# Optimization experiments

Measured on AMD Instinct MI355X. Metric: run time of the kernel, lower is better.

The kernel has to match this reference:

```python
import jax, jax.numpy as jnp
import numpy as np

D = 768

def setup_inputs() -> dict:
    key = jax.random.key(0)
    ks = jax.random.split(key, 12)
    inp = {
        "text_embeddings": jax.random.normal(ks[0], (8, 512, D), dtype=jnp.float32),
        "kb_emb": jax.random.normal(ks[1], (200000, D), dtype=jnp.float32),
        "W_ret": jax.random.normal(ks[2], (D, D), dtype=jnp.float32) * 0.02,
        "b_ret": jax.random.normal(ks[3], (D,), dtype=jnp.float32) * 0.02,
        "Ws1": jax.random.normal(ks[4], (2 * D, D), dtype=jnp.float32) * 0.02,
        "bs1": jax.random.normal(ks[5], (D,), dtype=jnp.float32) * 0.02,
        "Ws2": jax.random.normal(ks[6], (D, 1), dtype=jnp.float32) * 0.02,
        "bs2": jax.random.normal(ks[7], (1,), dtype=jnp.float32) * 0.02,
        "mention_sent": jax.random.randint(ks[8], (256,), 0, 8, dtype=jnp.int32),
        "mention_start": jax.random.randint(ks[9], (256,), 0, 480, dtype=jnp.int32),
        "mention_len": jax.random.randint(ks[10], (256,), 0, 31, dtype=jnp.int32),
        "top_k": 100,
    }
    return inp


def reference(text_embeddings, kb_emb, W_ret, b_ret, Ws1, bs1, Ws2, bs2,
              mention_sent, mention_start, mention_len, top_k):
    S = text_embeddings.shape[1]
    pos = jnp.arange(S, dtype=jnp.int32)
    # inclusive span [start, start+len] -> mask [M, S]
    mask = (pos[None, :] >= mention_start[:, None]) & (pos[None, :] <= (mention_start + mention_len)[:, None])
    maskf = mask.astype(text_embeddings.dtype)
    sent = text_embeddings[mention_sent]                       # [M, S, D]
    mention_emb = jnp.einsum('msd,ms->md', sent, maskf) / maskf.sum(1, keepdims=True)

    # entity_retriever linear, then KB dot-product retrieval of top 2k candidates
    query = mention_emb @ W_ret.T + b_ret                      # [M, D]
    sims = query @ kb_emb.T                                    # [M, N]
    _, cand_idx = jax.lax.top_k(sims, 2 * top_k)               # [M, 2k]
    cand_embs = kb_emb[cand_idx]                               # [M, 2k, D]

    # candidate_scorer: Linear(2D->D) on concat(mention, cand) + ReLU + Linear(D->1) + Sigmoid
    m_part = mention_emb @ Ws1[:D]                             # [M, D]
    c_part = jnp.einsum('mkd,de->mke', cand_embs, Ws1[D:])     # [M, 2k, D]
    h = jax.nn.relu(m_part[:, None, :] + c_part + bs1)
    scores = jax.nn.sigmoid(jnp.einsum('mke,eo->mko', h, Ws2)[..., 0] + bs2[0])  # [M, 2k]

    top_scores, ti = jax.lax.top_k(scores, top_k)              # [M, k]
    top_kb_idx = jnp.take_along_axis(cand_idx, ti, axis=1)
    return top_scores, top_kb_idx
```

## Files before the change

kernel.cpp:

```cpp
#include <hip/hip_runtime.h>
#include <cfloat>
#include <cmath>
#include <cstdint>

#define DD 768
#define MM 256
#define NKB 200000
#define SLEN 512
#define KK 200
#define TOPK 100
#define SURV_CAP 1024
#define RESC 232
#define THRC 2.70f
#define MAXMARK 32768
#define DELTA 4e-5
#define NET 12

typedef __attribute__((ext_vector_type(8))) short bf16x8;
typedef __attribute__((ext_vector_type(4))) float f32x4;

__device__ __forceinline__ unsigned short f2bf_rne(float x) {
  unsigned u = __float_as_uint(x);
  unsigned r = (u + 0x7FFFu + ((u >> 16) & 1u)) >> 16;
  return (unsigned short)r;
}
__device__ __forceinline__ float bf2f(unsigned short us) {
  return __uint_as_float(((unsigned)us) << 16);
}
__device__ __forceinline__ void splitbf(float x, unsigned short& hi, unsigned short& lo) {
  hi = f2bf_rne(x);
  lo = f2bf_rne(x - bf2f(hi));
}

__global__ __launch_bounds__(256) void k_prepT(
    const float* __restrict__ Wret, float* __restrict__ WretT) {
  __shared__ float tile[64][65];
  int e0 = blockIdx.x * 64, d0 = blockIdx.y * 64;
  int tid = threadIdx.x;
  int r = tid >> 6, cc = tid & 63;
  for (int i = 0; i < 64; i += 4)
    tile[r + i][cc] = Wret[(size_t)(e0 + r + i) * DD + d0 + cc];
  __syncthreads();
  for (int i = 0; i < 64; i += 4)
    WretT[(size_t)(d0 + r + i) * DD + e0 + cc] = tile[cc][r + i];
}

__global__ __launch_bounds__(256) void k_front(
    const float* __restrict__ text, const int* __restrict__ msent,
    const int* __restrict__ mstart, const int* __restrict__ mlen,
    const float* __restrict__ WretT, const float* __restrict__ bret,
    const float* __restrict__ Ws1,
    double* __restrict__ q64, unsigned short* __restrict__ qb16,
    float* __restrict__ tthr, double* __restrict__ mp64,
    float* __restrict__ mp32) {
  int m = blockIdx.x;
  __shared__ double sme[DD];
  __shared__ float snorm[256];
  int tid = threadIdx.x;
  {
    int sent = msent[m], st = mstart[m], ln = mlen[m];
    const float* base = text + (size_t)sent * SLEN * DD;
    for (int d = tid; d < DD; d += 256) {
      double acc = 0.0;
      for (int s = st; s <= st + ln; ++s) acc += (double)base[(size_t)s * DD + d];
      sme[d] = acc / (double)(ln + 1);
    }
  }
  __syncthreads();
  float nloc = 0.f;
  for (int e = tid; e < DD; e += 256) {
    double aq = (double)bret[e];
    double amp = 0.0;
    for (int d = 0; d < DD; ++d) {
      double md = sme[d];
      aq  += md * (double)WretT[(size_t)d * DD + e];
      amp += md * (double)Ws1[(size_t)d * DD + e];
    }
    q64[(size_t)m * DD + e] = aq;
    qb16[(size_t)m * DD + e] = f2bf_rne((float)aq);
    mp64[(size_t)m * DD + e] = amp;
    mp32[(size_t)m * DD + e] = (float)amp;
    nloc += (float)(aq * aq);
  }
  snorm[tid] = nloc; __syncthreads();
  for (int s = 128; s > 0; s >>= 1) {
    if (tid < s) snorm[tid] += snorm[tid + s];
    __syncthreads();
  }
  if (tid == 0) tthr[m] = THRC * sqrtf(snorm[0]);
}

__global__ __launch_bounds__(256) void k_prep(
    const float* __restrict__ Ws1, unsigned short* __restrict__ Bth,
    unsigned short* __restrict__ Btl) {
  int e = blockIdx.x;
  for (int k = threadIdx.x; k < DD; k += 256) {
    float x = Ws1[(size_t)(DD + k) * DD + e];
    unsigned short hi, lo;
    splitbf(x, hi, lo);
    Bth[(size_t)e * DD + k] = hi;
    Btl[(size_t)e * DD + k] = lo;
  }
}

__global__ __launch_bounds__(512) void k_sims_mfma(
    const unsigned short* __restrict__ qb, const float* __restrict__ kb,
    const float* __restrict__ tthr, int* __restrict__ gcnt,
    uint2* __restrict__ gcand) {
  __shared__ unsigned short Bs[2][64 * 64];
  __shared__ float sthr[256];
  int n0 = blockIdx.x * 64;
  int tid = threadIdx.x;
  int lane = tid & 63, w = tid >> 6;
  int h = lane >> 4, c = lane & 15;
  if (tid < 256) sthr[tid] = tthr[tid];
  f32x4 acc[2][4] = {};
  const int brow = n0 + (tid >> 3);
  const int bg   = tid & 7;
  const int bwoff = ((tid >> 3) * 128 + bg * 16) ^ (((tid >> 3) & 7) << 4);
  auto ldB = [&](int k0, float4 &d0, float4 &d1) {
    const float* s = kb + (size_t)brow * DD + k0 + bg * 8;
    d0 = *(const float4*)(s);
    d1 = *(const float4*)(s + 4);
  };
  auto stB = [&](int buf, const float4 &v0, const float4 &v1) {
    uint4 p;
    p.x = (unsigned)f2bf_rne(v0.x) | ((unsigned)f2bf_rne(v0.y) << 16);
    p.y = (unsigned)f2bf_rne(v0.z) | ((unsigned)f2bf_rne(v0.w) << 16);
    p.z = (unsigned)f2bf_rne(v1.x) | ((unsigned)f2bf_rne(v1.y) << 16);
    p.w = (unsigned)f2bf_rne(v1.z) | ((unsigned)f2bf_rne(v1.w) << 16);
    *(uint4*)((char*)Bs + buf * 8192 + bwoff) = p;
  };
  const unsigned short* qa0 = qb + (size_t)(w * 32 + c) * DD;
  const unsigned short* qa1 = qb + (size_t)(w * 32 + 16 + c) * DD;
  float4 c0, c1, p1a, p1b, p2a, p2b;
  ldB(0, c0, c1);
  stB(0, c0, c1);
  ldB(64, p1a, p1b);
  ldB(128, p2a, p2b);
  __syncthreads();
#pragma unroll
  for (int s = 0; s < 12; ++s) {
    int cur = s & 1;
    int k0 = s * 64;
    if (s + 1 < 12) stB(cur ^ 1, p1a, p1b);
    p1a = p2a; p1b = p2b;
    if (s + 3 < 12) ldB((s + 3) * 64, p2a, p2b);
    bf16x8 a00 = *(const bf16x8*)(qa0 + k0 + h * 8);
    bf16x8 a10 = *(const bf16x8*)(qa1 + k0 + h * 8);
    bf16x8 a01 = *(const bf16x8*)(qa0 + k0 + 32 + h * 8);
    bf16x8 a11 = *(const bf16x8*)(qa1 + k0 + 32 + h * 8);
#pragma unroll
    for (int nf = 0; nf < 4; ++nf) {
      int n = nf * 16 + c;
      int off = (n * 128 + h * 16) ^ ((n & 7) << 4);
      bf16x8 b = *(bf16x8*)((char*)Bs + cur * 8192 + off);
      acc[0][nf] = __builtin_amdgcn_mfma_f32_16x16x32_bf16(a00, b, acc[0][nf], 0, 0, 0);
      acc[1][nf] = __builtin_amdgcn_mfma_f32_16x16x32_bf16(a10, b, acc[1][nf], 0, 0, 0);
    }
#pragma unroll
    for (int nf = 0; nf < 4; ++nf) {
      int n = nf * 16 + c;
      int off = (n * 128 + 64 + h * 16) ^ ((n & 7) << 4);
      bf16x8 b = *(bf16x8*)((char*)Bs + cur * 8192 + off);
      acc[0][nf] = __builtin_amdgcn_mfma_f32_16x16x32_bf16(a01, b, acc[0][nf], 0, 0, 0);
      acc[1][nf] = __builtin_amdgcn_mfma_f32_16x16x32_bf16(a11, b, acc[1][nf], 0, 0, 0);
    }
    __syncthreads();
  }
#pragma unroll
  for (int mf = 0; mf < 2; ++mf)
#pragma unroll
    for (int nf = 0; nf < 4; ++nf)
#pragma unroll
      for (int r = 0; r < 4; ++r) {
        int row = w * 32 + mf * 16 + h * 4 + r;
        int col = n0 + nf * 16 + c;
        float v = acc[mf][nf][r];
        if (v > sthr[row]) {
          int p = atomicAdd(&gcnt[row], 1);
          if (p < SURV_CAP) gcand[(size_t)row * SURV_CAP + p] = make_uint2(__float_as_uint(v), (unsigned)col);
        }
      }
}

__global__ __launch_bounds__(256) void k_select(
    const uint2* __restrict__ gcand, const int* __restrict__ gcnt,
    const float* __restrict__ kb, const double* __restrict__ q64,
    int* __restrict__ cidx) {
  int m = blockIdx.x;
  __shared__ float skf[SURV_CAP];
  __shared__ int   sidx[SURV_CAP];
  __shared__ double sq[DD];
  __shared__ double skey[256];
  __shared__ int    skidx[256];
  int tid = threadIdx.x;
  int cnt = gcnt[m]; if (cnt > SURV_CAP) cnt = SURV_CAP;
  for (int d = tid; d < DD; d += 256) sq[d] = q64[(size_t)m * DD + d];
  for (int i = tid; i < SURV_CAP; i += 256) {
    if (i < cnt) {
      uint2 v = gcand[(size_t)m * SURV_CAP + i];
      skf[i] = __uint_as_float(v.x);
      sidx[i] = (int)v.y;
    } else { skf[i] = -FLT_MAX; sidx[i] = 0x7fffffff; }
  }
  __syncthreads();
  for (int k = 2; k <= SURV_CAP; k <<= 1) {
    for (int j = k >> 1; j > 0; j >>= 1) {
      for (int i = tid; i < SURV_CAP; i += 256) {
        int l = i ^ j;
        if (l > i) {
          float ka = skf[i], kb2 = skf[l];
          int ia = sidx[i], ib = sidx[l];
          bool lBefore = (kb2 > ka) || (kb2 == ka && ib < ia);
          bool iBefore = (ka > kb2) || (ka == kb2 && ia < ib);
          bool dir = ((i & k) == 0);
          bool sw = dir ? lBefore : iBefore;
          if (sw) { skf[i] = kb2; skf[l] = ka; sidx[i] = ib; sidx[l] = ia; }
        }
      }
      __syncthreads();
    }
  }
  int lane = tid & 63, wv = tid >> 6;
  for (int cpos = wv; cpos < RESC; cpos += 4) {
    int ci = sidx[cpos];
    double s;
    if (ci < NKB) {
      const float* krow = kb + (size_t)ci * DD;
      double acc = 0.0;
      for (int d = lane; d < DD; d += 64) acc += sq[d] * (double)krow[d];
      for (int off2 = 32; off2 > 0; off2 >>= 1) acc += __shfl_down(acc, off2, 64);
      s = acc;
    } else s = -INFINITY;
    if (lane == 0) { skey[cpos] = s; skidx[cpos] = ci; }
  }
  if (tid >= RESC && tid < 256) { skey[tid] = -INFINITY; skidx[tid] = 0x7fffffff; }
  __syncthreads();
  for (int k = 2; k <= 256; k <<= 1) {
    for (int j = k >> 1; j > 0; j >>= 1) {
      int i = tid, l = i ^ j;
      if (l > i) {
        double ka = skey[i], kb2 = skey[l];
        int ia = skidx[i], ib = skidx[l];
        bool lBefore = (kb2 > ka) || (kb2 == ka && ib < ia);
        bool iBefore = (ka > kb2) || (ka == kb2 && ia < ib);
        bool dir = ((i & k) == 0);
        bool sw = dir ? lBefore : iBefore;
        if (sw) { skey[i] = kb2; skey[l] = ka; skidx[i] = ib; skidx[l] = ia; }
      }
      __syncthreads();
    }
  }
  for (int cc = tid; cc < KK; cc += 256) {
    int v = skidx[cc];
    cidx[(size_t)m * KK + cc] = (v < NKB) ? v : 0;
  }
}

__global__ __launch_bounds__(256) void k_score2(
    const float* __restrict__ kb, const int* __restrict__ cidx,
    const float* __restrict__ mp32, const unsigned short* __restrict__ Bth,
    const unsigned short* __restrict__ Btl, const float* __restrict__ bs1,
    const float* __restrict__ Ws2, float* __restrict__ gpart) {
  __shared__ unsigned short Ah[256 * 32], Al[256 * 32];
  __shared__ unsigned short Bh[64 * 32], Bl[64 * 32];
  __shared__ float smp[3][64], sb1v[64], sw2v[64];
  __shared__ int srow[256];
  int p = blockIdx.x;
  int x = p & 7, j = p >> 3;
  int ct = x + 8 * (j / NET), et = j % NET;
  int r0 = ct * 256, e0 = et * 64;
  int tid = threadIdx.x, lane = tid & 63, w = tid >> 6;
  int h = lane >> 4, c = lane & 15;
  srow[tid] = cidx[r0 + tid];
  int m0 = r0 / KK;
  int mm1 = (m0 + 1 < MM) ? m0 + 1 : MM - 1;
  int mm2 = (m0 + 2 < MM) ? m0 + 2 : MM - 1;
  if (tid < 64) {
    smp[0][tid] = mp32[(size_t)m0 * DD + e0 + tid];
    smp[1][tid] = mp32[(size_t)mm1 * DD + e0 + tid];
    smp[2][tid] = mp32[(size_t)mm2 * DD + e0 + tid];
    sb1v[tid] = bs1[e0 + tid];
    sw2v[tid] = Ws2[e0 + tid];
  }
  __syncthreads();
  const float* aaddr[8];
#pragma unroll
  for (int it = 0; it < 8; ++it) {
    int idx = tid + it * 256;
    int rr = idx >> 3, f4 = idx & 7;
    aaddr[it] = kb + (size_t)srow[rr] * DD + f4 * 4;
  }
  const int be = tid >> 2, bk8 = tid & 3;
  const unsigned short* bhaddr = Bth + (size_t)(e0 + be) * DD + bk8 * 8;
  const unsigned short* bladdr = Btl + (size_t)(e0 + be) * DD + bk8 * 8;
  float4 pa[8];
  uint4 pbh, pbl;
#pragma unroll
  for (int it = 0; it < 8; ++it) pa[it] = *(const float4*)(aaddr[it]);
  pbh = *(const uint4*)(bhaddr);
  pbl = *(const uint4*)(bladdr);
  f32x4 acc[4][4] = {};
  for (int k0 = 0; k0 < DD; k0 += 32) {
    __syncthreads();
#pragma unroll
    for (int it = 0; it < 8; ++it) {
      int idx = tid + it * 256;
      int rr = idx >> 3, f4 = idx & 7;
      float4 v = pa[it];
      unsigned short h0, h1, h2, h3, l0, l1, l2, l3;
      splitbf(v.x, h0, l0); splitbf(v.y, h1, l1);
      splitbf(v.z, h2, l2); splitbf(v.w, h3, l3);
      uint2 ph, pl;
      ph.x = (unsigned)h0 | ((unsigned)h1 << 16); ph.y = (unsigned)h2 | ((unsigned)h3 << 16);
      pl.x = (unsigned)l0 | ((unsigned)l1 << 16); pl.y = (unsigned)l2 | ((unsigned)l3 << 16);
      int off = (rr * 64 + f4 * 8) ^ ((rr & 7) << 4);
      *(uint2*)((char*)Ah + off) = ph;
      *(uint2*)((char*)Al + off) = pl;
    }
    {
      int off = (be * 64 + bk8 * 16) ^ ((be & 7) << 4);
      *(uint4*)((char*)Bh + off) = pbh;
      *(uint4*)((char*)Bl + off) = pbl;
    }
    if (k0 + 32 < DD) {
#pragma unroll
      for (int it = 0; it < 8; ++it) pa[it] = *(const float4*)(aaddr[it] + k0 + 32);
      pbh = *(const uint4*)(bhaddr + k0 + 32);
      pbl = *(const uint4*)(bladdr + k0 + 32);
    }
    __syncthreads();
    bf16x8 ah[4], al[4];
#pragma unroll
    for (int mf = 0; mf < 4; ++mf) {
      int rr = w * 64 + mf * 16 + c;
      int off = (rr * 64 + h * 16) ^ ((rr & 7) << 4);
      ah[mf] = *(bf16x8*)((char*)Ah + off);
      al[mf] = *(bf16x8*)((char*)Al + off);
    }
#pragma unroll
    for (int nf = 0; nf < 4; ++nf) {
      int e = nf * 16 + c;
      int off = (e * 64 + h * 16) ^ ((e & 7) << 4);
      bf16x8 bh = *(bf16x8*)((char*)Bh + off);
      bf16x8 bl = *(bf16x8*)((char*)Bl + off);
#pragma unroll
      for (int mf = 0; mf < 4; ++mf) {
        acc[mf][nf] = __builtin_amdgcn_mfma_f32_16x16x32_bf16(ah[mf], bh, acc[mf][nf], 0, 0, 0);
        acc[mf][nf] = __builtin_amdgcn_mfma_f32_16x16x32_bf16(ah[mf], bl, acc[mf][nf], 0, 0, 0);
        acc[mf][nf] = __builtin_amdgcn_mfma_f32_16x16x32_bf16(al[mf], bh, acc[mf][nf], 0, 0, 0);
      }
    }
  }
  int bnd1 = (m0 + 1) * KK, bnd2 = (m0 + 2) * KK;
#pragma unroll
  for (int mf = 0; mf < 4; ++mf) {
    float zp[4] = {0.f, 0.f, 0.f, 0.f};
#pragma unroll
    for (int nf = 0; nf < 4; ++nf) {
      int el = nf * 16 + c;
      float b1v = sb1v[el], w2v = sw2v[el];
#pragma unroll
      for (int r = 0; r < 4; ++r) {
        int rowg = r0 + w * 64 + mf * 16 + h * 4 + r;
        int sel = (rowg >= bnd1) + (rowg >= bnd2);
        float hh = acc[mf][nf][r] + smp[sel][el] + b1v;
        if (hh > 0.f) zp[r] += hh * w2v;
      }
    }
#pragma unroll
    for (int r = 0; r < 4; ++r) {
      float v = zp[r];
      v += __shfl_xor(v, 1, 64);
      v += __shfl_xor(v, 2, 64);
      v += __shfl_xor(v, 4, 64);
      v += __shfl_xor(v, 8, 64);
      if (c == 0)
        gpart[(size_t)(r0 + w * 64 + mf * 16 + h * 4 + r) * NET + et] = v;
    }
  }
}

__global__ __launch_bounds__(256) void k_mark(
    const float* __restrict__ gpart, const float* __restrict__ bs2,
    double* __restrict__ z64, int* __restrict__ marks, int* __restrict__ mcnt) {
  int m = blockIdx.x;
  __shared__ double sk[256];
  __shared__ int sp[256];
  __shared__ int flag[256];
  int tid = threadIdx.x;
  flag[tid] = 0;
  if (tid < KK) {
    double s = 0.0;
#pragma unroll
    for (int i = 0; i < NET; ++i) s += (double)gpart[(size_t)(m * KK + tid) * NET + i];
    s += (double)bs2[0];
    z64[(size_t)m * KK + tid] = s;
    sk[tid] = s; sp[tid] = tid;
  } else { sk[tid] = -INFINITY; sp[tid] = 0x7fffffff; }
  __syncthreads();
  for (int k = 2; k <= 256; k <<= 1) {
    for (int j = k >> 1; j > 0; j >>= 1) {
      int i = tid, l = i ^ j;
      if (l > i) {
        double ka = sk[i], kb2 = sk[l];
        int ia = sp[i], ib = sp[l];
        bool lBefore = (kb2 > ka) || (kb2 == ka && ib < ia);
        bool iBefore = (ka > kb2) || (ka == kb2 && ia < ib);
        bool dir = ((i & k) == 0);
        bool sw = dir ? lBefore : iBefore;
        if (sw) { sk[i] = kb2; sk[l] = ka; sp[i] = ib; sp[l] = ia; }
      }
      __syncthreads();
    }
  }
  if (tid <= 120) {
    if (sk[tid] - sk[tid + 1] < DELTA) {
      flag[tid] = 1;
      atomicExch(&flag[tid + 1], 1);
    }
  }
  __syncthreads();
  if (tid <= 121 && flag[tid]) {
    int p = atomicAdd(mcnt, 1);
    if (p < MAXMARK) marks[p] = m * KK + sp[tid];
  }
}

__global__ __launch_bounds__(256) void k_rescore(
    const float* __restrict__ kb, const int* __restrict__ cidx,
    const double* __restrict__ mp64, const float* __restrict__ Ws1,
    const float* __restrict__ bs1, const float* __restrict__ Ws2,
    const float* __restrict__ bs2, const int* __restrict__ marks,
    const int* __restrict__ mcnt, double* __restrict__ z64) {
  int cnt = *mcnt; if (cnt > MAXMARK) cnt = MAXMARK;
  __shared__ float sc[DD];
  __shared__ double sred[256];
  int tid = threadIdx.x;
  for (int it = blockIdx.x; it < cnt; it += gridDim.x) {
    int r = marks[it];
    int m = r / KK;
    int row = cidx[r];
    for (int d = tid; d < DD; d += 256) sc[d] = kb[(size_t)row * DD + d];
    __syncthreads();
    double pz = 0.0;
    for (int e = tid; e < DD; e += 256) {
      double a = 0.0;
      for (int d = 0; d < DD; ++d) a += (double)sc[d] * (double)Ws1[(size_t)(DD + d) * DD + e];
      double hv = mp64[(size_t)m * DD + e] + a + (double)bs1[e];
      if (hv > 0) pz += hv * (double)Ws2[e];
    }
    sred[tid] = pz; __syncthreads();
    for (int s = 128; s > 0; s >>= 1) { if (tid < s) sred[tid] += sred[tid + s]; __syncthreads(); }
    if (tid == 0) z64[r] = sred[0] + (double)bs2[0];
    __syncthreads();
  }
}

__global__ __launch_bounds__(256) void k_final(
    const double* __restrict__ z64, const int* __restrict__ cidx, float* __restrict__ out) {
  int m = blockIdx.x;
  __shared__ double sk[256];
  __shared__ int sp[256];
  int tid = threadIdx.x;
  if (tid < KK) { sk[tid] = z64[(size_t)m * KK + tid]; sp[tid] = tid; }
  else { sk[tid] = -INFINITY; sp[tid] = 0x7fffffff; }
  __syncthreads();
  for (int k = 2; k <= 256; k <<= 1) {
    for (int j = k >> 1; j > 0; j >>= 1) {
      int i = tid, l = i ^ j;
      if (l > i) {
        double ka = sk[i], kb2 = sk[l];
        int ia = sp[i], ib = sp[l];
        bool lBefore = (kb2 > ka) || (kb2 == ka && ib < ia);
        bool iBefore = (ka > kb2) || (ka == kb2 && ia < ib);
        bool dir = ((i & k) == 0);
        bool sw = dir ? lBefore : iBefore;
        if (sw) { sk[i] = kb2; sk[l] = ka; sp[i] = ib; sp[l] = ia; }
      }
      __syncthreads();
    }
  }
  if (tid < TOPK) {
    double z = sk[tid];
    out[(size_t)m * TOPK + tid] = (float)(1.0 / (1.0 + exp(-z)));
    out[(size_t)MM * TOPK + (size_t)m * TOPK + tid] = (float)cidx[(size_t)m * KK + sp[tid]];
  }
}

extern "C" void kernel_launch(void* const* d_in, const int* in_sizes, int n_in,
                              void* d_out, int out_size, void* d_ws, size_t ws_size,
                              hipStream_t stream) {
  const float* text  = (const float*)d_in[0];
  const float* kb    = (const float*)d_in[1];
  const float* Wret  = (const float*)d_in[2];
  const float* bret  = (const float*)d_in[3];
  const float* Ws1   = (const float*)d_in[4];
  const float* bs1   = (const float*)d_in[5];
  const float* Ws2   = (const float*)d_in[6];
  const float* bs2   = (const float*)d_in[7];
  const int* msent   = (const int*)d_in[8];
  const int* mstart  = (const int*)d_in[9];
  const int* mlen    = (const int*)d_in[10];
  float* out = (float*)d_out;

  char* ws = (char*)d_ws;
  size_t off = 0;
  auto alloc = [&](size_t bytes) -> void* {
    void* p = ws + off;
    off = (off + bytes + 255) & ~(size_t)255;
    return p;
  };
  double* q64  = (double*)alloc((size_t)MM * DD * 8);
  unsigned short* qb16 = (unsigned short*)alloc((size_t)MM * DD * 2);
  float*  tthr = (float*) alloc((size_t)MM * 4);
  double* mp64 = (double*)alloc((size_t)MM * DD * 8);
  float*  mp32 = (float*) alloc((size_t)MM * DD * 4);
  int*    cidx = (int*)   alloc((size_t)MM * KK * 4);
  double* z64  = (double*)alloc((size_t)MM * KK * 8);
  float*  gpart = (float*)alloc((size_t)MM * KK * NET * 4);
  int*    marks = (int*)  alloc((size_t)MAXMARK * 4);
  int*    mcnt  = (int*)  alloc(256);
  int*    gcnt  = (int*)  alloc((size_t)MM * 4);
  uint2*  gcand = (uint2*)alloc((size_t)MM * SURV_CAP * 8);
  unsigned short* Bth = (unsigned short*)alloc((size_t)DD * DD * 2);
  unsigned short* Btl = (unsigned short*)alloc((size_t)DD * DD * 2);
  float*  WretT = (float*)alloc((size_t)DD * DD * 4);
  (void)ws_size;

  dim3 gt(DD / 64, DD / 64);
  k_prepT<<<gt, 256, 0, stream>>>(Wret, WretT);
  k_prep<<<DD, 256, 0, stream>>>(Ws1, Bth, Btl);
  k_front<<<MM, 256, 0, stream>>>(text, msent, mstart, mlen, WretT, bret, Ws1,
                                  q64, qb16, tthr, mp64, mp32);

  hipMemsetAsync(gcnt, 0, (size_t)MM * 4, stream);
  k_sims_mfma<<<NKB / 64, 512, 0, stream>>>(qb16, kb, tthr, gcnt, gcand);
  k_select<<<MM, 256, 0, stream>>>(gcand, gcnt, kb, q64, cidx);

  k_score2<<<(MM * KK / 256) * NET, 256, 0, stream>>>(kb, cidx, mp32, Bth, Btl, bs1, Ws2, gpart);
  hipMemsetAsync(mcnt, 0, 4, stream);
  k_mark<<<MM, 256, 0, stream>>>(gpart, bs2, z64, marks, mcnt);
  k_rescore<<<2048, 256, 0, stream>>>(kb, cidx, mp64, Ws1, bs1, Ws2, bs2, marks, mcnt, z64);
  k_final<<<MM, 256, 0, stream>>>(z64, cidx, out);
}
```

Before: 1.287 ms.

## Halve sims block to 4 waves, each covering 64 query rows with 32-wide K steps

The KB similarity GEMM block shrinks from 8 waves to 4, and each wave now covers 64 mention rows (4 M-fragments) instead of 32. The K loop steps by 32 instead of 64, halving the shared-memory B tile. Each B fragment read from LDS now feeds four MFMAs instead of two, which raises register reuse and cuts LDS traffic per FLOP. The cost is more accumulator registers per thread, and twice as many barrier-separated iterations.

```diff
diff --git a/kernel.cpp b/kernel.cpp
--- a/kernel.cpp
+++ b/kernel.cpp
@@ -103,23 +103,23 @@
   }
 }
 
-__global__ __launch_bounds__(512) void k_sims_mfma(
+__global__ __launch_bounds__(256) void k_sims_mfma(
     const unsigned short* __restrict__ qb, const float* __restrict__ kb,
     const float* __restrict__ tthr, int* __restrict__ gcnt,
     uint2* __restrict__ gcand) {
-  __shared__ unsigned short Bs[2][64 * 64];
+  __shared__ unsigned short Bs[2][64 * 32];
   __shared__ float sthr[256];
   int n0 = blockIdx.x * 64;
   int tid = threadIdx.x;
   int lane = tid & 63, w = tid >> 6;
   int h = lane >> 4, c = lane & 15;
-  if (tid < 256) sthr[tid] = tthr[tid];
-  f32x4 acc[2][4] = {};
-  const int brow = n0 + (tid >> 3);
-  const int bg   = tid & 7;
-  const int bwoff = ((tid >> 3) * 128 + bg * 16) ^ (((tid >> 3) & 7) << 4);
+  sthr[tid] = tthr[tid];
+  f32x4 acc[4][4] = {};
+  const int brow = n0 + (tid >> 2);
+  const int bkg  = (tid & 3) * 8;
+  const int bwoff = ((tid >> 2) * 64 + bkg * 2) ^ (((tid >> 2) & 7) << 4);
   auto ldB = [&](int k0, float4 &d0, float4 &d1) {
-    const float* s = kb + (size_t)brow * DD + k0 + bg * 8;
+    const float* s = kb + (size_t)brow * DD + k0 + bkg;
     d0 = *(const float4*)(s);
     d1 = *(const float4*)(s + 4);
   };
@@ -129,52 +129,47 @@
     p.y = (unsigned)f2bf_rne(v0.z) | ((unsigned)f2bf_rne(v0.w) << 16);
     p.z = (unsigned)f2bf_rne(v1.x) | ((unsigned)f2bf_rne(v1.y) << 16);
     p.w = (unsigned)f2bf_rne(v1.z) | ((unsigned)f2bf_rne(v1.w) << 16);
-    *(uint4*)((char*)Bs + buf * 8192 + bwoff) = p;
+    *(uint4*)((char*)Bs + buf * 4096 + bwoff) = p;
   };
-  const unsigned short* qa0 = qb + (size_t)(w * 32 + c) * DD;
-  const unsigned short* qa1 = qb + (size_t)(w * 32 + 16 + c) * DD;
+  const unsigned short* qa[4];
+#pragma unroll
+  for (int mf = 0; mf < 4; ++mf)
+    qa[mf] = qb + (size_t)(w * 64 + mf * 16 + c) * DD;
   float4 c0, c1, p1a, p1b, p2a, p2b;
   ldB(0, c0, c1);
   stB(0, c0, c1);
-  ldB(64, p1a, p1b);
-  ldB(128, p2a, p2b);
-  __syncthreads();
-#pragma unroll
-  for (int s = 0; s < 12; ++s) {
+  ldB(32, p1a, p1b);
+  ldB(64, p2a, p2b);
+  __syncthreads();
+#pragma unroll
+  for (int s = 0; s < 24; ++s) {
     int cur = s & 1;
-    int k0 = s * 64;
-    if (s + 1 < 12) stB(cur ^ 1, p1a, p1b);
+    int k0 = s * 32;
+    if (s + 1 < 24) stB(cur ^ 1, p1a, p1b);
     p1a = p2a; p1b = p2b;
-    if (s + 3 < 12) ldB((s + 3) * 64, p2a, p2b);
-    bf16x8 a00 = *(const bf16x8*)(qa0 + k0 + h * 8);
-    bf16x8 a10 = *(const bf16x8*)(qa1 + k0 + h * 8);
-    bf16x8 a01 = *(const bf16x8*)(qa0 + k0 + 32 + h * 8);
-    bf16x8 a11 = *(const bf16x8*)(qa1 + k0 + 32 + h * 8);
+    if (s + 3 < 24) ldB((s + 3) * 32, p2a, p2b);
+    bf16x8 a[4];
+#pragma unroll
+    for (int mf = 0; mf < 4; ++mf)
+      a[mf] = *(const bf16x8*)(qa[mf] + k0 + h * 8);
 #pragma unroll
     for (int nf = 0; nf < 4; ++nf) {
       int n = nf * 16 + c;
-      int off = (n * 128 + h * 16) ^ ((n & 7) << 4);
-      bf16x8 b = *(bf16x8*)((char*)Bs + cur * 8192 + off);
-      acc[0][nf] = __builtin_amdgcn_mfma_f32_16x16x32_bf16(a00, b, acc[0][nf], 0, 0, 0);
-      acc[1][nf] = __builtin_amdgcn_mfma_f32_16x16x32_bf16(a10, b, acc[1][nf], 0, 0, 0);
-    }
-#pragma unroll
-    for (int nf = 0; nf < 4; ++nf) {
-      int n = nf * 16 + c;
-      int off = (n * 128 + 64 + h * 16) ^ ((n & 7) << 4);
-      bf16x8 b = *(bf16x8*)((char*)Bs + cur * 8192 + off);
-      acc[0][nf] = __builtin_amdgcn_mfma_f32_16x16x32_bf16(a01, b, acc[0][nf], 0, 0, 0);
-      acc[1][nf] = __builtin_amdgcn_mfma_f32_16x16x32_bf16(a11, b, acc[1][nf], 0, 0, 0);
+      int off = (n * 64 + h * 16) ^ ((n & 7) << 4);
+      bf16x8 b = *(bf16x8*)((char*)Bs + cur * 4096 + off);
+#pragma unroll
+      for (int mf = 0; mf < 4; ++mf)
+        acc[mf][nf] = __builtin_amdgcn_mfma_f32_16x16x32_bf16(a[mf], b, acc[mf][nf], 0, 0, 0);
     }
     __syncthreads();
   }
 #pragma unroll
-  for (int mf = 0; mf < 2; ++mf)
+  for (int mf = 0; mf < 4; ++mf)
 #pragma unroll
     for (int nf = 0; nf < 4; ++nf)
 #pragma unroll
       for (int r = 0; r < 4; ++r) {
-        int row = w * 32 + mf * 16 + h * 4 + r;
+        int row = w * 64 + mf * 16 + h * 4 + r;
         int col = n0 + nf * 16 + c;
         float v = acc[mf][nf][r];
         if (v > sthr[row]) {
@@ -536,7 +531,7 @@
                                   q64, qb16, tthr, mp64, mp32);
 
   hipMemsetAsync(gcnt, 0, (size_t)MM * 4, stream);
-  k_sims_mfma<<<NKB / 64, 512, 0, stream>>>(qb16, kb, tthr, gcnt, gcand);
+  k_sims_mfma<<<NKB / 64, 256, 0, stream>>>(qb16, kb, tthr, gcnt, gcand);
   k_select<<<MM, 256, 0, stream>>>(gcand, gcnt, kb, q64, cidx);
 
   k_score2<<<(MM * KK / 256) * NET, 256, 0, stream>>>(kb, cidx, mp32, Bth, Btl, bs1, Ws2, gpart);
```

Result: slower. 1.352 ms (+5.1%).
